# Performance work log

Hardware: AMD Instinct MI355X
Metric: run time of the kernel (lower is better)

The kernel has to match this reference:

```python
import jax, jax.numpy as jnp
import numpy as np
import math

D_MODEL = 1024
N_HEADS = 16
FFN_DIM = 4096
B, L = 8, 1024
LN_EPS = 1e-5


def setup_inputs() -> dict:
    key = jax.random.key(0)
    ks = jax.random.split(key, 16)
    s = 1.0 / math.sqrt(D_MODEL)
    sf = 1.0 / math.sqrt(FFN_DIM)
    # weights stored [in, out] (transposed vs torch nn.Linear)
    return {
        "x": jax.random.normal(ks[0], (B, L, D_MODEL), dtype=jnp.float32),
        "Wq": jax.random.normal(ks[1], (D_MODEL, D_MODEL), dtype=jnp.float32) * s,
        "bq": jnp.zeros((D_MODEL,), jnp.float32),
        "Wk": jax.random.normal(ks[2], (D_MODEL, D_MODEL), dtype=jnp.float32) * s,
        "bk": jnp.zeros((D_MODEL,), jnp.float32),
        "Wv": jax.random.normal(ks[3], (D_MODEL, D_MODEL), dtype=jnp.float32) * s,
        "bv": jnp.zeros((D_MODEL,), jnp.float32),
        "Wo": jax.random.normal(ks[4], (D_MODEL, D_MODEL), dtype=jnp.float32) * s,
        "bo": jnp.zeros((D_MODEL,), jnp.float32),
        "W1": jax.random.normal(ks[5], (D_MODEL, FFN_DIM), dtype=jnp.float32) * s,
        "b1": jnp.zeros((FFN_DIM,), jnp.float32),
        "W2": jax.random.normal(ks[6], (FFN_DIM, D_MODEL), dtype=jnp.float32) * sf,
        "b2": jnp.zeros((D_MODEL,), jnp.float32),
        "gamma": jnp.ones((D_MODEL,), jnp.float32),
        "beta": jnp.zeros((D_MODEL,), jnp.float32),
    }


def reference(x, Wq, bq, Wk, bk, Wv, bv, Wo, bo, W1, b1, W2, b2, gamma, beta):
    Bb, Ll, D = x.shape
    H = N_HEADS
    E = D // H
    scale = 1.0 / math.sqrt(E)
    # multi-head attention (dropout is identity in eval)
    q = (x @ Wq + bq).reshape(Bb, Ll, H, E)
    k = (x @ Wk + bk).reshape(Bb, Ll, H, E)
    v = (x @ Wv + bv).reshape(Bb, Ll, H, E)
    scores = jnp.einsum('blhe,bshe->bhls', q, k)  # [B,H,L,L]
    A = jax.nn.softmax(scale * scores, axis=-1)
    ctx = jnp.einsum('bhls,bshd->blhd', A, v).reshape(Bb, Ll, D)
    attn_out = ctx @ Wo + bo
    x = x + attn_out
    # FFN: conv1d kernel_size=1 == pointwise linear; exact (erf) GELU as in F.gelu
    h = jax.nn.gelu(x @ W1 + b1, approximate=False)
    x = x + (h @ W2 + b2)
    # LayerNorm
    mu = jnp.mean(x, axis=-1, keepdims=True)
    var = jnp.mean(jnp.square(x - mu), axis=-1, keepdims=True)
    out = (x - mu) * jax.lax.rsqrt(var + LN_EPS) * gamma + beta
    return out
```

## Files before the change

### kernel.cpp

```cpp
#include <hip/hip_runtime.h>
#include <cmath>

typedef __attribute__((ext_vector_type(8))) _Float16 half8;
typedef __attribute__((ext_vector_type(4))) _Float16 half4;
typedef __attribute__((ext_vector_type(4))) float f32x4;

__device__ __forceinline__ void glds16(const void* g, void* l) {
  __builtin_amdgcn_global_load_lds(
      (__attribute__((address_space(1))) const void*)g,
      (__attribute__((address_space(3))) void*)l, 16, 0, 0);
}

__device__ __forceinline__ float fast_erf(float x) {
  float ax = fabsf(x);
  float t = 1.0f / (1.0f + 0.3275911f * ax);
  float y = t * (0.254829592f +
            t * (-0.284496736f +
            t * (1.421413741f +
            t * (-1.453152027f + t * 1.061405429f))));
  float r = 1.0f - y * __expf(-ax * ax);
  return copysignf(r, x);
}

__global__ __launch_bounds__(256) void k_cvt(const float* __restrict__ in,
                                             _Float16* __restrict__ out) {
  int i = (blockIdx.x * 256 + threadIdx.x) * 8;
  const f32x4* p = (const f32x4*)(in + i);
  f32x4 a = p[0], b = p[1];
  half8 h;
  h[0] = (_Float16)a[0]; h[1] = (_Float16)a[1]; h[2] = (_Float16)a[2]; h[3] = (_Float16)a[3];
  h[4] = (_Float16)b[0]; h[5] = (_Float16)b[1]; h[6] = (_Float16)b[2]; h[7] = (_Float16)b[3];
  *(half8*)(out + i) = h;
}

__global__ __launch_bounds__(256) void k_wt(const float* __restrict__ W,
                                            _Float16* __restrict__ Wt, int K, int N) {
  __shared__ float t[32][33];
  int x = threadIdx.x & 31, y4 = (threadIdx.x >> 5) << 2;
  int n0 = blockIdx.x << 5, k0 = blockIdx.y << 5;
#pragma unroll
  for (int r = 0; r < 4; ++r) t[y4 + r][x] = W[(size_t)(k0 + y4 + r) * N + n0 + x];
  __syncthreads();
#pragma unroll
  for (int r = 0; r < 4; ++r) Wt[(size_t)(n0 + y4 + r) * K + k0 + x] = (_Float16)t[x][y4 + r];
}

__global__ void k_biascat(const float* __restrict__ a, const float* __restrict__ b,
                          const float* __restrict__ c, float* __restrict__ o) {
  int i = blockIdx.x * 256 + threadIdx.x;
  const float* s = i < 1024 ? a : (i < 2048 ? b : c);
  o[i] = s[i & 1023];
}

template <int BM, int EPI>
__global__ __launch_bounds__(512, 2) void k_gemm8(
    const _Float16* __restrict__ A, const _Float16* __restrict__ Bt,
    const float* __restrict__ bias, const float* __restrict__ res,
    float* __restrict__ outf, _Float16* __restrict__ outh, int M, int N, int K) {
  constexpr int MR = BM / 32;
  constexpr int MH2 = MR / 2;
  constexpr int AL = BM * 64;
  constexpr int BL = 256 * 64;
  constexpr int ABYTES = BM * 128;
  constexpr int BBYTES = 256 * 128;
  constexpr int AB2 = 2 * ABYTES;
  __shared__ _Float16 lds[2 * (AL + BL)];
  const char* ldsc = (const char*)lds;

  const int tid = threadIdx.x;
  const int lane = tid & 63;
  const int w = tid >> 6, wr = w >> 2, wc = w & 3;
  const int l15 = lane & 15, grp = lane >> 4;

  const int gx = gridDim.x;
  const int nwg = gx * gridDim.y;
  const int lid = blockIdx.y * gx + blockIdx.x;
  const int wid = (lid & 7) * (nwg >> 3) + (lid >> 3);
  const int m0 = (wid / gx) * BM, n0 = (wid % gx) * 256;

  const int m2 = (l15 >> 2) & 1, m01 = l15 & 3;
  const int chunk0 = (m2 << 2) | (grp ^ m01);
  const int aoff0 = wr * 2048 + l15 * 128 + chunk0 * 16;
  const int aoff1 = aoff0 ^ 64;
  const int boff0 = wc * 2048 + l15 * 128 + chunk0 * 16;
  const int boff1 = boff0 ^ 64;

  const int srow = tid >> 3;
  const int scs8 = ((tid & 7) ^ (srow & 7)) * 8;
  const int NK = K >> 6;

  f32x4 acc[MR][4] = {};
  half8 af[MH2][2], bf[2][2];

#define STG_A(J, MHH, KN)                                                      \
  _Pragma("unroll") for (int s = 0; s < BM / 128; ++s)                         \
      glds16(A + (size_t)(m0 + (MHH) * (BM / 2) + s * 64 + srow) * K +         \
                 (size_t)(KN)*64 + scs8,                                       \
             lds + (J)*AL + ((MHH) * (BM / 2) + s * 64) * 64 + tid * 8);
#define STG_B(J, NHH, KN)                                                      \
  _Pragma("unroll") for (int s = 0; s < 2; ++s)                                \
      glds16(Bt + (size_t)(n0 + (NHH)*128 + s * 64 + srow) * K +               \
                  (size_t)(KN)*64 + scs8,                                      \
             lds + 2 * AL + (J)*BL + ((NHH)*128 + s * 64) * 64 + tid * 8);

#define VM_C asm volatile("s_waitcnt vmcnt(2)" ::: "memory")
#define VM_NONE

#define PHASE(J, MHQ, NHQ, RA, RB, STGSTMT, VMSTMT)                            \
  {                                                                            \
    if constexpr (RA) {                                                        \
      _Pragma("unroll") for (int i = 0; i < MH2; ++i) {                        \
        af[i][0] = *(const half8*)(ldsc + (J)*ABYTES +                         \
                                   ((MHQ)*MH2 + i) * 4096 + aoff0);            \
        af[i][1] = *(const half8*)(ldsc + (J)*ABYTES +                         \
                                   ((MHQ)*MH2 + i) * 4096 + aoff1);            \
      }                                                                        \
    }                                                                          \
    if constexpr (RB) {                                                        \
      _Pragma("unroll") for (int n = 0; n < 2; ++n) {                          \
        bf[n][0] = *(const half8*)(ldsc + AB2 + (J)*BBYTES +                   \
                                   ((NHQ)*2 + n) * 8192 + boff0);              \
        bf[n][1] = *(const half8*)(ldsc + AB2 + (J)*BBYTES +                   \
                                   ((NHQ)*2 + n) * 8192 + boff1);              \
      }                                                                        \
    }                                                                          \
    STGSTMT;                                                                   \
    __builtin_amdgcn_s_barrier();                                              \
    asm volatile("s_waitcnt lgkmcnt(0)");                                      \
    __builtin_amdgcn_sched_barrier(0);                                         \
    __builtin_amdgcn_s_setprio(1);                                             \
    _Pragma("unroll") for (int ks = 0; ks < 2; ++ks)                           \
        _Pragma("unroll") for (int i = 0; i < MH2; ++i)                        \
            _Pragma("unroll") for (int n = 0; n < 2; ++n)                      \
                acc[(MHQ)*MH2 + i][(NHQ)*2 + n] =                              \
                    __builtin_amdgcn_mfma_f32_16x16x32_f16(                    \
                        af[i][ks], bf[n][ks], acc[(MHQ)*MH2 + i][(NHQ)*2 + n], \
                        0, 0, 0);                                              \
    __builtin_amdgcn_s_setprio(0);                                             \
    VMSTMT;                                                                    \
    __builtin_amdgcn_s_barrier();                                              \
  }

#define KTILE(J, KT)                                                           \
  {                                                                            \
    const int kn_ = ((KT) + 1 < NK) ? (KT) + 1 : NK - 1;                       \
    const int kn2_ = ((KT) + 2 < NK) ? (KT) + 2 : NK - 1;                      \
    PHASE(J, 0, 0, true, true, STG_A(1 - (J), 0, kn_), VM_NONE)                \
    PHASE(J, 0, 1, false, true, STG_A(1 - (J), 1, kn_), VM_NONE)               \
    PHASE(J, 1, 1, true, false, STG_B(1 - (J), 0, kn_), VM_NONE)               \
    PHASE(J, 1, 0, false, true, STG_B(J, 1, kn2_), VM_C)                       \
  }

  STG_A(0, 0, 0) STG_A(0, 1, 0) STG_B(0, 0, 0) STG_B(0, 1, 0)
  STG_B(1, 1, 1)
  VM_C;
  __builtin_amdgcn_s_barrier();

#pragma unroll 1
  for (int kt = 0; kt < NK; kt += 2) {
    KTILE(0, kt)
    KTILE(1, kt + 1)
  }
  asm volatile("s_waitcnt vmcnt(0)" ::: "memory");
#undef KTILE
#undef PHASE
#undef VM_C
#undef VM_NONE
#undef STG_A
#undef STG_B

  float bcol[4];
#pragma unroll
  for (int n = 0; n < 4; ++n) bcol[n] = bias[n0 + (n * 4 + wc) * 16 + l15];
#pragma unroll
  for (int m = 0; m < MR; ++m) {
#pragma unroll
    for (int rr = 0; rr < 4; ++rr) {
      const size_t row = m0 + (m * 2 + wr) * 16 + grp * 4 + rr;
#pragma unroll
      for (int n = 0; n < 4; ++n) {
        const int col = n0 + (n * 4 + wc) * 16 + l15;
        float v = acc[m][n][rr] + bcol[n];
        const size_t idx = row * N + col;
        if (EPI == 0) {
          outh[idx] = (_Float16)v;
        } else if (EPI == 1) {
          float t2 = v + res[idx];
          outf[idx] = t2;
          outh[idx] = (_Float16)t2;
        } else if (EPI == 2) {
          float g = 0.5f * v * (1.0f + fast_erf(v * 0.70710678118654752f));
          outh[idx] = (_Float16)g;
        } else {
          outf[idx] = v + res[idx];
        }
      }
    }
  }
}

template <int EPI>
__global__ __launch_bounds__(512, 2) void k_gemmf(
    const _Float16* __restrict__ A, const _Float16* __restrict__ Bt,
    const float* __restrict__ bias, const void* __restrict__ res,
    float* __restrict__ outf, _Float16* __restrict__ outh, int M, int N, int K) {
  constexpr int AL = 256 * 64, BL = 128 * 64;
  constexpr int ABY = 32768, BBY = 16384, BBASE = 3 * ABY;
  __shared__ _Float16 lds[3 * (AL + BL)];
  const char* ldsc = (const char*)lds;

  const int tid = threadIdx.x;
  const int lane = tid & 63;
  const int w = tid >> 6, wr = w >> 1, wc = w & 1;
  const int l15 = lane & 15, grp = lane >> 4;

  const int gx = gridDim.x;
  const int nwg = gx * gridDim.y;
  const int lid = blockIdx.y * gx + blockIdx.x;
  const int wid = (lid & 7) * (nwg >> 3) + (lid >> 3);
  const int m0 = (wid / gx) * 256, n0 = (wid % gx) * 128;

  const int m2 = (l15 >> 2) & 1, m01 = l15 & 3;
  const int c0 = ((m2 << 2) | (grp ^ m01)) * 16;
  const int aoff0 = wr * 2048 + l15 * 128 + c0;
  const int aoff1 = aoff0 ^ 64;
  const int boff0 = wc * 2048 + l15 * 128 + c0;
  const int boff1 = boff0 ^ 64;

  const int srow = tid >> 3;
  const int scs8 = ((tid & 7) ^ (srow & 7)) * 8;
  const int NK = K >> 6;

  const _Float16* aG = A + (size_t)(m0 + srow) * K + scs8;
  const _Float16* bG = Bt + (size_t)(n0 + srow) * K + scs8;

  f32x4 acc[4][4] = {};

#define FSTG_A(JJ, HH, KN)                                                     \
  _Pragma("unroll") for (int s = 0; s < 2; ++s)                                \
      glds16(aG + (size_t)((HH)*128 + s * 64) * K + (size_t)(KN)*64,           \
             lds + (JJ)*AL + ((HH)*128 + s * 64) * 64 + tid * 8);
#define FSTG_B(JJ, HH, KN)                                                     \
  glds16(bG + (size_t)((HH)*64) * K + (size_t)(KN)*64,                         \
         lds + 3 * AL + (JJ)*BL + (HH)*64 * 64 + tid * 8);

#define FPHASE(PA, PB, AO, BO, STGSTMT, VMSTMT)                                \
  {                                                                            \
    half8 af_[4], bf_[4];                                                      \
    _Pragma("unroll") for (int m = 0; m < 4; ++m)                              \
        af_[m] = *(const half8*)((PA) + m * 8192 + (AO));                      \
    _Pragma("unroll") for (int n = 0; n < 4; ++n)                              \
        bf_[n] = *(const half8*)((PB) + n * 4096 + (BO));                      \
    STGSTMT;                                                                   \
    __builtin_amdgcn_s_barrier();                                              \
    asm volatile("s_waitcnt lgkmcnt(0)");                                      \
    __builtin_amdgcn_sched_barrier(0);                                         \
    __builtin_amdgcn_s_setprio(1);                                             \
    _Pragma("unroll") for (int m = 0; m < 4; ++m)                              \
        _Pragma("unroll") for (int n = 0; n < 4; ++n)                          \
            acc[m][n] = __builtin_amdgcn_mfma_f32_16x16x32_f16(                \
                af_[m], bf_[n], acc[m][n], 0, 0, 0);                           \
    __builtin_amdgcn_s_setprio(0);                                             \
    VMSTMT;                                                                    \
    __builtin_amdgcn_s_barrier();                                              \
  }

  FSTG_A(0, 0, 0) FSTG_A(0, 1, 0) FSTG_B(0, 0, 0) FSTG_B(0, 1, 0)
  FSTG_A(1, 0, 1) FSTG_A(1, 1, 1) FSTG_B(1, 0, 1) FSTG_B(1, 1, 1)
  asm volatile("s_waitcnt vmcnt(6)" ::: "memory");
  __builtin_amdgcn_s_barrier();

  int j = 0, j2 = 2;
#pragma unroll 1
  for (int kt = 0; kt < NK; ++kt) {
    const int kn = (kt + 2 < NK) ? kt + 2 : NK - 1;
    const char* pa = ldsc + j * ABY;
    const char* pb = ldsc + BBASE + j * BBY;
    FPHASE(pa, pb, aoff0, boff0, { FSTG_A(j2, 0, kn) FSTG_B(j2, 0, kn) }, )
    FPHASE(pa, pb, aoff1, boff1, { FSTG_A(j2, 1, kn) FSTG_B(j2, 1, kn) },
           asm volatile("s_waitcnt vmcnt(6)" ::: "memory");)
    j = (j == 2) ? 0 : j + 1;
    j2 = (j2 == 2) ? 0 : j2 + 1;
  }
  asm volatile("s_waitcnt vmcnt(0)" ::: "memory");
#undef FPHASE
#undef FSTG_A
#undef FSTG_B

  float bcol[4];
#pragma unroll
  for (int n = 0; n < 4; ++n) bcol[n] = bias[n0 + (n * 2 + wc) * 16 + l15];
#pragma unroll
  for (int m = 0; m < 4; ++m) {
#pragma unroll
    for (int rr = 0; rr < 4; ++rr) {
      const size_t row = m0 + (m * 4 + wr) * 16 + grp * 4 + rr;
#pragma unroll
      for (int n = 0; n < 4; ++n) {
        const int col = n0 + (n * 2 + wc) * 16 + l15;
        float v = acc[m][n][rr] + bcol[n];
        const size_t idx = row * N + col;
        if (EPI == 0) {
          outh[idx] = (_Float16)v;
        } else if (EPI == 1) {
          float t2 = v + ((const float*)res)[idx];
          outh[idx] = (_Float16)t2;
        } else if (EPI == 2) {
          float g = 0.5f * v * (1.0f + fast_erf(v * 0.70710678118654752f));
          outh[idx] = (_Float16)g;
        } else {
          float t2 = v + (float)((const _Float16*)res)[idx];
          outf[idx] = t2;
        }
      }
    }
  }
}

__global__ __launch_bounds__(256) void k_vt(const _Float16* __restrict__ qkv,
                                            _Float16* __restrict__ Vt) {
  __shared__ _Float16 t[64 * 66];
  const int tid = threadIdx.x;
  const int bh = blockIdx.y, b = bh >> 4, h = bh & 15;
  const int s0 = blockIdx.x << 6;
#pragma unroll
  for (int p = 0; p < 2; ++p) {
    int lin = p * 256 + tid;
    int s = lin >> 3, c8 = lin & 7;
    half8 v = *(const half8*)&qkv[(size_t)(b * 1024 + s0 + s) * 3072 + 2048 + h * 64 + c8 * 8];
    union { half8 h8; unsigned u[4]; } u;
    u.h8 = v;
    unsigned* d = (unsigned*)&t[s * 66 + c8 * 8];
#pragma unroll
    for (int k = 0; k < 4; ++k) d[k] = u.u[k];
  }
  __syncthreads();
#pragma unroll
  for (int p = 0; p < 2; ++p) {
    int lin = p * 256 + tid;
    int e = lin >> 3, c8 = lin & 7;
    half8 v;
#pragma unroll
    for (int j = 0; j < 8; ++j) v[j] = t[(c8 * 8 + j) * 66 + e];
    *(half8*)&Vt[(size_t)(bh * 64 + e) * 1024 + s0 + c8 * 8] = v;
  }
}

__global__ __launch_bounds__(256) void k_attn(const _Float16* __restrict__ qkv,
                                              const _Float16* __restrict__ Vt,
                                              _Float16* __restrict__ ctx) {
  __shared__ _Float16 Ks[128 * 64];
  __shared__ _Float16 Vs[64 * 128];
  __shared__ _Float16 Ps[4][16 * 136];
  const int tid = threadIdx.x;
  const int lane = tid & 63, w = tid >> 6;
  const int l15 = lane & 15, grp = lane >> 4;
  const int bh = blockIdx.y, b = bh >> 4, h = bh & 15;
  const int q0 = blockIdx.x << 6;
  const float CSC = 0.125f * 1.44269504088896f;

  half8 qf[2];
  {
    const _Float16* qp = qkv + (size_t)(b * 1024 + q0 + w * 16 + l15) * 3072 + h * 64 + grp * 8;
    qf[0] = *(const half8*)qp;
    qf[1] = *(const half8*)(qp + 32);
  }
  f32x4 octx[4] = {};
  float mrun = -1e30f, lrun = 0.f;

  for (int kt = 0; kt < 8; ++kt) {
    const int s0 = kt * 128;
#pragma unroll
    for (int i = 0; i < 4; ++i) {
      {
        int srow = i * 32 + (tid >> 3);
        int c8 = (tid & 7) ^ (srow & 7);
        glds16(qkv + (size_t)(b * 1024 + s0 + srow) * 3072 + 1024 + h * 64 + c8 * 8,
               Ks + w * 512 + i * 2048);
      }
      {
        int erow = i * 16 + (tid >> 4);
        int c16 = (tid & 15) ^ (erow & 7);
        glds16(Vt + (size_t)(bh * 64 + erow) * 1024 + s0 + c16 * 8,
               Vs + w * 512 + i * 2048);
      }
    }
    __syncthreads();
    f32x4 sacc[8] = {};
#pragma unroll
    for (int ks = 0; ks < 2; ++ks)
#pragma unroll
      for (int f = 0; f < 8; ++f) {
        int srow = f * 16 + l15;
        half8 kf = *(const half8*)&Ks[srow * 64 + ((ks * 32 + grp * 8) ^ ((srow & 7) * 8))];
        sacc[f] = __builtin_amdgcn_mfma_f32_16x16x32_f16(kf, qf[ks], sacc[f], 0, 0, 0);
      }
    float sv[8][4];
    float tmax = -1e30f;
#pragma unroll
    for (int f = 0; f < 8; ++f)
#pragma unroll
      for (int r = 0; r < 4; ++r) {
        float v = sacc[f][r] * CSC;
        sv[f][r] = v;
        tmax = fmaxf(tmax, v);
      }
    tmax = fmaxf(tmax, __shfl_xor(tmax, 16));
    tmax = fmaxf(tmax, __shfl_xor(tmax, 32));
    float mnew = fmaxf(mrun, tmax);
    float corr = exp2f(mrun - mnew);
    float tsum = 0.f;
#pragma unroll
    for (int f = 0; f < 8; ++f)
#pragma unroll
      for (int r = 0; r < 4; ++r) {
        float pv = exp2f(sv[f][r] - mnew);
        sv[f][r] = pv;
        tsum += pv;
      }
    tsum += __shfl_xor(tsum, 16);
    tsum += __shfl_xor(tsum, 32);
    lrun = lrun * corr + tsum;
    mrun = mnew;
#pragma unroll
    for (int r = 0; r < 4; ++r) {
      float cq = __shfl(corr, (lane & 48) + grp * 4 + r);
#pragma unroll
      for (int jf = 0; jf < 4; ++jf) octx[jf][r] *= cq;
    }
#pragma unroll
    for (int f = 0; f < 8; ++f) {
      half4 pk;
      pk[0] = (_Float16)sv[f][0]; pk[1] = (_Float16)sv[f][1];
      pk[2] = (_Float16)sv[f][2]; pk[3] = (_Float16)sv[f][3];
      *(half4*)&Ps[w][l15 * 136 + f * 16 + grp * 4] = pk;
    }
#pragma unroll
    for (int ks2 = 0; ks2 < 4; ++ks2) {
      half8 pa = *(const half8*)&Ps[w][l15 * 136 + ks2 * 32 + grp * 8];
#pragma unroll
      for (int jf = 0; jf < 4; ++jf) {
        int erow = jf * 16 + l15;
        half8 vb = *(const half8*)&Vs[erow * 128 + ((ks2 * 32 + grp * 8) ^ ((erow & 7) * 8))];
        octx[jf] = __builtin_amdgcn_mfma_f32_16x16x32_f16(pa, vb, octx[jf], 0, 0, 0);
      }
    }
    __syncthreads();
  }
#pragma unroll
  for (int r = 0; r < 4; ++r) {
    float lq = __shfl(lrun, (lane & 48) + grp * 4 + r);
    float inv = 1.0f / lq;
    const size_t row = b * 1024 + q0 + w * 16 + grp * 4 + r;
#pragma unroll
    for (int jf = 0; jf < 4; ++jf)
      ctx[row * 1024 + h * 64 + jf * 16 + l15] = (_Float16)(octx[jf][r] * inv);
  }
}

__global__ __launch_bounds__(256) void k_ln(const float* xin, const float* __restrict__ gamma,
                                            const float* __restrict__ beta, float* out) {
  __shared__ float red[8];
  const int tid = threadIdx.x;
  const size_t row = blockIdx.x;
  f32x4 v = *(const f32x4*)&xin[row * 1024 + tid * 4];
  float s = v[0] + v[1] + v[2] + v[3];
  float s2 = v[0] * v[0] + v[1] * v[1] + v[2] * v[2] + v[3] * v[3];
#pragma unroll
  for (int o = 32; o >= 1; o >>= 1) {
    s += __shfl_xor(s, o);
    s2 += __shfl_xor(s2, o);
  }
  if ((tid & 63) == 0) { red[tid >> 6] = s; red[4 + (tid >> 6)] = s2; }
  __syncthreads();
  s = red[0] + red[1] + red[2] + red[3];
  s2 = red[4] + red[5] + red[6] + red[7];
  float mu = s * (1.0f / 1024.0f);
  float var = s2 * (1.0f / 1024.0f) - mu * mu;
  float rs = rsqrtf(var + 1e-5f);
  f32x4 g = *(const f32x4*)&gamma[tid * 4];
  f32x4 bt = *(const f32x4*)&beta[tid * 4];
  f32x4 o4;
#pragma unroll
  for (int r = 0; r < 4; ++r) o4[r] = (v[r] - mu) * rs * g[r] + bt[r];
  *(f32x4*)&out[row * 1024 + tid * 4] = o4;
}

extern "C" void kernel_launch(void* const* d_in, const int* in_sizes, int n_in,
                              void* d_out, int out_size, void* d_ws, size_t ws_size,
                              hipStream_t stream) {
  (void)in_sizes; (void)n_in; (void)out_size; (void)ws_size;
  const float* x  = (const float*)d_in[0];
  const float* Wq = (const float*)d_in[1];  const float* bq = (const float*)d_in[2];
  const float* Wk = (const float*)d_in[3];  const float* bk = (const float*)d_in[4];
  const float* Wv = (const float*)d_in[5];  const float* bv = (const float*)d_in[6];
  const float* Wo = (const float*)d_in[7];  const float* bo = (const float*)d_in[8];
  const float* W1 = (const float*)d_in[9];  const float* b1 = (const float*)d_in[10];
  const float* W2 = (const float*)d_in[11]; const float* b2 = (const float*)d_in[12];
  const float* gamma = (const float*)d_in[13];
  const float* beta  = (const float*)d_in[14];
  float* out = (float*)d_out;

  char* p = (char*)d_ws;
  _Float16* xb    = (_Float16*)p;  p += (size_t)16 << 20;
  _Float16* qkv   = (_Float16*)p;
  _Float16* hbuf  = (_Float16*)p;  p += (size_t)48 << 20;
  _Float16* Vt    = (_Float16*)p;  p += (size_t)16 << 20;
  _Float16* Wqkvt = (_Float16*)p;  p += (size_t)3072 * 1024 * 2;
  _Float16* Wot   = (_Float16*)p;  p += (size_t)1024 * 1024 * 2;
  _Float16* W1t   = (_Float16*)p;  p += (size_t)4096 * 1024 * 2;
  _Float16* W2t   = (_Float16*)p;  p += (size_t)4096 * 1024 * 2;
  float*    bqkv  = (float*)p;     p += (size_t)3072 * 4;
  _Float16* x1b   = (_Float16*)p;  p += (size_t)16 << 20;
  _Float16* ctx   = xb;

  k_cvt<<<4096, 256, 0, stream>>>(x, xb);
  k_wt<<<dim3(32, 32), 256, 0, stream>>>(Wq, Wqkvt, 1024, 1024);
  k_wt<<<dim3(32, 32), 256, 0, stream>>>(Wk, Wqkvt + 1024 * 1024, 1024, 1024);
  k_wt<<<dim3(32, 32), 256, 0, stream>>>(Wv, Wqkvt + 2048 * 1024, 1024, 1024);
  k_wt<<<dim3(32, 32), 256, 0, stream>>>(Wo, Wot, 1024, 1024);
  k_wt<<<dim3(128, 32), 256, 0, stream>>>(W1, W1t, 1024, 4096);
  k_wt<<<dim3(32, 128), 256, 0, stream>>>(W2, W2t, 4096, 1024);
  k_biascat<<<12, 256, 0, stream>>>(bq, bk, bv, bqkv);

  k_gemmf<0><<<dim3(24, 32), 512, 0, stream>>>(xb, Wqkvt, bqkv, nullptr, nullptr, qkv,
                                               8192, 3072, 1024);
  k_vt<<<dim3(16, 128), 256, 0, stream>>>(qkv, Vt);
  k_attn<<<dim3(16, 128), 256, 0, stream>>>(qkv, Vt, ctx);
  k_gemmf<1><<<dim3(8, 32), 512, 0, stream>>>(ctx, Wot, bo, x, nullptr, x1b,
                                              8192, 1024, 1024);
  k_gemm8<256, 2><<<dim3(16, 32), 512, 0, stream>>>(x1b, W1t, b1, nullptr, nullptr, hbuf,
                                                    8192, 4096, 1024);
  k_gemmf<4><<<dim3(8, 32), 512, 0, stream>>>(hbuf, W2t, b2, x1b, out, nullptr,
                                              8192, 1024, 4096);
  k_ln<<<8192, 256, 0, stream>>>(out, gamma, beta, out);
}
```

Baseline: 360.3 us.

## Fuse V transpose into QKV GEMM epilogue and double query rows per attention block

The QKV GEMM gets a new epilogue mode that writes the V columns directly in transposed [b,h,e,s] layout, so the separate k_vt transpose kernel and its extra pass over V are removed. The attention kernel now handles 128 query rows per block (two 64-row sub-tiles), reusing each K/V tile loaded into LDS twice and halving the grid. The order of the A/B staging loads in the GEMM pipeline phases is also swapped. Costs: the transposed V stores are 8-byte scattered writes, and attention has more registers per thread and fewer blocks in flight.

After: 361.0 us. Within noise of the previous version (+0.2%).

```diff
diff --git a/kernel.cpp b/kernel.cpp
--- a/kernel.cpp
+++ b/kernel.cpp
@@ -146,12 +146,12 @@
     const int kn_ = ((KT) + 1 < NK) ? (KT) + 1 : NK - 1;                       \
     const int kn2_ = ((KT) + 2 < NK) ? (KT) + 2 : NK - 1;                      \
     PHASE(J, 0, 0, true, true, STG_A(1 - (J), 0, kn_), VM_NONE)                \
-    PHASE(J, 0, 1, false, true, STG_A(1 - (J), 1, kn_), VM_NONE)               \
-    PHASE(J, 1, 1, true, false, STG_B(1 - (J), 0, kn_), VM_NONE)               \
+    PHASE(J, 0, 1, false, true, STG_B(1 - (J), 0, kn_), VM_NONE)               \
+    PHASE(J, 1, 1, true, false, STG_A(1 - (J), 1, kn_), VM_NONE)               \
     PHASE(J, 1, 0, false, true, STG_B(J, 1, kn2_), VM_C)                       \
   }
 
-  STG_A(0, 0, 0) STG_A(0, 1, 0) STG_B(0, 0, 0) STG_B(0, 1, 0)
+  STG_A(0, 0, 0) STG_B(0, 0, 0) STG_A(0, 1, 0) STG_B(0, 1, 0)
   STG_B(1, 1, 1)
   VM_C;
   __builtin_amdgcn_s_barrier();
@@ -290,6 +290,30 @@
   float bcol[4];
 #pragma unroll
   for (int n = 0; n < 4; ++n) bcol[n] = bias[n0 + (n * 2 + wc) * 16 + l15];
+  if (EPI == 5) {
+    _Float16* vt = (_Float16*)outf;
+#pragma unroll
+    for (int m = 0; m < 4; ++m) {
+#pragma unroll
+      for (int n = 0; n < 4; ++n) {
+        const int col = n0 + (n * 2 + wc) * 16 + l15;
+        const size_t row0 = m0 + (m * 4 + wr) * 16 + grp * 4;
+        if (col < 2048) {
+#pragma unroll
+          for (int rr = 0; rr < 4; ++rr)
+            outh[(row0 + rr) * (size_t)N + col] = (_Float16)(acc[m][n][rr] + bcol[n]);
+        } else {
+          const int b = (int)(row0 >> 10), s = (int)(row0 & 1023);
+          const int cv = col - 2048, hh = cv >> 6, e = cv & 63;
+          half4 pk;
+#pragma unroll
+          for (int rr = 0; rr < 4; ++rr) pk[rr] = (_Float16)(acc[m][n][rr] + bcol[n]);
+          *(half4*)&vt[((size_t)((b << 4) | hh) * 64 + e) * 1024 + s] = pk;
+        }
+      }
+    }
+    return;
+  }
 #pragma unroll
   for (int m = 0; m < 4; ++m) {
 #pragma unroll
@@ -317,35 +341,6 @@
   }
 }
 
-__global__ __launch_bounds__(256) void k_vt(const _Float16* __restrict__ qkv,
-                                            _Float16* __restrict__ Vt) {
-  __shared__ _Float16 t[64 * 66];
-  const int tid = threadIdx.x;
-  const int bh = blockIdx.y, b = bh >> 4, h = bh & 15;
-  const int s0 = blockIdx.x << 6;
-#pragma unroll
-  for (int p = 0; p < 2; ++p) {
-    int lin = p * 256 + tid;
-    int s = lin >> 3, c8 = lin & 7;
-    half8 v = *(const half8*)&qkv[(size_t)(b * 1024 + s0 + s) * 3072 + 2048 + h * 64 + c8 * 8];
-    union { half8 h8; unsigned u[4]; } u;
-    u.h8 = v;
-    unsigned* d = (unsigned*)&t[s * 66 + c8 * 8];
-#pragma unroll
-    for (int k = 0; k < 4; ++k) d[k] = u.u[k];
-  }
-  __syncthreads();
-#pragma unroll
-  for (int p = 0; p < 2; ++p) {
-    int lin = p * 256 + tid;
-    int e = lin >> 3, c8 = lin & 7;
-    half8 v;
-#pragma unroll
-    for (int j = 0; j < 8; ++j) v[j] = t[(c8 * 8 + j) * 66 + e];
-    *(half8*)&Vt[(size_t)(bh * 64 + e) * 1024 + s0 + c8 * 8] = v;
-  }
-}
-
 __global__ __launch_bounds__(256) void k_attn(const _Float16* __restrict__ qkv,
                                               const _Float16* __restrict__ Vt,
                                               _Float16* __restrict__ ctx) {
@@ -356,17 +351,19 @@
   const int lane = tid & 63, w = tid >> 6;
   const int l15 = lane & 15, grp = lane >> 4;
   const int bh = blockIdx.y, b = bh >> 4, h = bh & 15;
-  const int q0 = blockIdx.x << 6;
+  const int q0 = blockIdx.x << 7;
   const float CSC = 0.125f * 1.44269504088896f;
 
-  half8 qf[2];
-  {
-    const _Float16* qp = qkv + (size_t)(b * 1024 + q0 + w * 16 + l15) * 3072 + h * 64 + grp * 8;
-    qf[0] = *(const half8*)qp;
-    qf[1] = *(const half8*)(qp + 32);
-  }
-  f32x4 octx[4] = {};
-  float mrun = -1e30f, lrun = 0.f;
+  half8 qf[2][2];
+#pragma unroll
+  for (int qs = 0; qs < 2; ++qs) {
+    const _Float16* qp =
+        qkv + (size_t)(b * 1024 + q0 + qs * 64 + w * 16 + l15) * 3072 + h * 64 + grp * 8;
+    qf[qs][0] = *(const half8*)qp;
+    qf[qs][1] = *(const half8*)(qp + 32);
+  }
+  f32x4 octx[2][4] = {};
+  float mrun[2] = {-1e30f, -1e30f}, lrun[2] = {0.f, 0.f};
 
   for (int kt = 0; kt < 8; ++kt) {
     const int s0 = kt * 128;
@@ -386,75 +383,81 @@
       }
     }
     __syncthreads();
-    f32x4 sacc[8] = {};
-#pragma unroll
-    for (int ks = 0; ks < 2; ++ks)
+#pragma unroll
+    for (int qs = 0; qs < 2; ++qs) {
+      f32x4 sacc[8] = {};
+#pragma unroll
+      for (int ks = 0; ks < 2; ++ks)
+#pragma unroll
+        for (int f = 0; f < 8; ++f) {
+          int srow = f * 16 + l15;
+          half8 kf = *(const half8*)&Ks[srow * 64 + ((ks * 32 + grp * 8) ^ ((srow & 7) * 8))];
+          sacc[f] = __builtin_amdgcn_mfma_f32_16x16x32_f16(kf, qf[qs][ks], sacc[f], 0, 0, 0);
+        }
+      float sv[8][4];
+      float tmax = -1e30f;
+#pragma unroll
+      for (int f = 0; f < 8; ++f)
+#pragma unroll
+        for (int r = 0; r < 4; ++r) {
+          float v = sacc[f][r] * CSC;
+          sv[f][r] = v;
+          tmax = fmaxf(tmax, v);
+        }
+      tmax = fmaxf(tmax, __shfl_xor(tmax, 16));
+      tmax = fmaxf(tmax, __shfl_xor(tmax, 32));
+      float mnew = fmaxf(mrun[qs], tmax);
+      float corr = exp2f(mrun[qs] - mnew);
+      float tsum = 0.f;
+#pragma unroll
+      for (int f = 0; f < 8; ++f)
+#pragma unroll
+        for (int r = 0; r < 4; ++r) {
+          float pv = exp2f(sv[f][r] - mnew);
+          sv[f][r] = pv;
+          tsum += pv;
+        }
+      tsum += __shfl_xor(tsum, 16);
+      tsum += __shfl_xor(tsum, 32);
+      lrun[qs] = lrun[qs] * corr + tsum;
+      mrun[qs] = mnew;
+#pragma unroll
+      for (int r = 0; r < 4; ++r) {
+        float cq = __shfl(corr, (lane & 48) + grp * 4 + r);
+#pragma unroll
+        for (int jf = 0; jf < 4; ++jf) octx[qs][jf][r] *= cq;
+      }
 #pragma unroll
       for (int f = 0; f < 8; ++f) {
-        int srow = f * 16 + l15;
-        half8 kf = *(const half8*)&Ks[srow * 64 + ((ks * 32 + grp * 8) ^ ((srow & 7) * 8))];
-        sacc[f] = __builtin_amdgcn_mfma_f32_16x16x32_f16(kf, qf[ks], sacc[f], 0, 0, 0);
-      }
-    float sv[8][4];
-    float tmax = -1e30f;
-#pragma unroll
-    for (int f = 0; f < 8; ++f)
-#pragma unroll
-      for (int r = 0; r < 4; ++r) {
-        float v = sacc[f][r] * CSC;
-        sv[f][r] = v;
-        tmax = fmaxf(tmax, v);
-      }
-    tmax = fmaxf(tmax, __shfl_xor(tmax, 16));
-    tmax = fmaxf(tmax, __shfl_xor(tmax, 32));
-    float mnew = fmaxf(mrun, tmax);
-    float corr = exp2f(mrun - mnew);
-    float tsum = 0.f;
-#pragma unroll
-    for (int f = 0; f < 8; ++f)
-#pragma unroll
-      for (int r = 0; r < 4; ++r) {
-        float pv = exp2f(sv[f][r] - mnew);
-        sv[f][r] = pv;
-        tsum += pv;
-      }
-    tsum += __shfl_xor(tsum, 16);
-    tsum += __shfl_xor(tsum, 32);
-    lrun = lrun * corr + tsum;
-    mrun = mnew;
-#pragma unroll
-    for (int r = 0; r < 4; ++r) {
-      float cq = __shfl(corr, (lane & 48) + grp * 4 + r);
-#pragma unroll
-      for (int jf = 0; jf < 4; ++jf) octx[jf][r] *= cq;
-    }
-#pragma unroll
-    for (int f = 0; f < 8; ++f) {
-      half4 pk;
-      pk[0] = (_Float16)sv[f][0]; pk[1] = (_Float16)sv[f][1];
-      pk[2] = (_Float16)sv[f][2]; pk[3] = (_Float16)sv[f][3];
-      *(half4*)&Ps[w][l15 * 136 + f * 16 + grp * 4] = pk;
-    }
-#pragma unroll
-    for (int ks2 = 0; ks2 < 4; ++ks2) {
-      half8 pa = *(const half8*)&Ps[w][l15 * 136 + ks2 * 32 + grp * 8];
-#pragma unroll
-      for (int jf = 0; jf < 4; ++jf) {
-        int erow = jf * 16 + l15;
-        half8 vb = *(const half8*)&Vs[erow * 128 + ((ks2 * 32 + grp * 8) ^ ((erow & 7) * 8))];
-        octx[jf] = __builtin_amdgcn_mfma_f32_16x16x32_f16(pa, vb, octx[jf], 0, 0, 0);
+        half4 pk;
+        pk[0] = (_Float16)sv[f][0]; pk[1] = (_Float16)sv[f][1];
+        pk[2] = (_Float16)sv[f][2]; pk[3] = (_Float16)sv[f][3];
+        *(half4*)&Ps[w][l15 * 136 + f * 16 + grp * 4] = pk;
+      }
+#pragma unroll
+      for (int ks2 = 0; ks2 < 4; ++ks2) {
+        half8 pa = *(const half8*)&Ps[w][l15 * 136 + ks2 * 32 + grp * 8];
+#pragma unroll
+        for (int jf = 0; jf < 4; ++jf) {
+          int erow = jf * 16 + l15;
+          half8 vb = *(const half8*)&Vs[erow * 128 + ((ks2 * 32 + grp * 8) ^ ((erow & 7) * 8))];
+          octx[qs][jf] = __builtin_amdgcn_mfma_f32_16x16x32_f16(pa, vb, octx[qs][jf], 0, 0, 0);
+        }
       }
     }
     __syncthreads();
   }
 #pragma unroll
-  for (int r = 0; r < 4; ++r) {
-    float lq = __shfl(lrun, (lane & 48) + grp * 4 + r);
-    float inv = 1.0f / lq;
-    const size_t row = b * 1024 + q0 + w * 16 + grp * 4 + r;
-#pragma unroll
-    for (int jf = 0; jf < 4; ++jf)
-      ctx[row * 1024 + h * 64 + jf * 16 + l15] = (_Float16)(octx[jf][r] * inv);
+  for (int qs = 0; qs < 2; ++qs) {
+#pragma unroll
+    for (int r = 0; r < 4; ++r) {
+      float lq = __shfl(lrun[qs], (lane & 48) + grp * 4 + r);
+      float inv = 1.0f / lq;
+      const size_t row = b * 1024 + q0 + qs * 64 + w * 16 + grp * 4 + r;
+#pragma unroll
+      for (int jf = 0; jf < 4; ++jf)
+        ctx[row * 1024 + h * 64 + jf * 16 + l15] = (_Float16)(octx[qs][jf][r] * inv);
+    }
   }
 }
 
@@ -523,10 +526,9 @@
   k_wt<<<dim3(32, 128), 256, 0, stream>>>(W2, W2t, 4096, 1024);
   k_biascat<<<12, 256, 0, stream>>>(bq, bk, bv, bqkv);
 
-  k_gemmf<0><<<dim3(24, 32), 512, 0, stream>>>(xb, Wqkvt, bqkv, nullptr, nullptr, qkv,
+  k_gemmf<5><<<dim3(24, 32), 512, 0, stream>>>(xb, Wqkvt, bqkv, nullptr, (float*)Vt, qkv,
                                                8192, 3072, 1024);
-  k_vt<<<dim3(16, 128), 256, 0, stream>>>(qkv, Vt);
-  k_attn<<<dim3(16, 128), 256, 0, stream>>>(qkv, Vt, ctx);
+  k_attn<<<dim3(8, 128), 256, 0, stream>>>(qkv, Vt, ctx);
   k_gemmf<1><<<dim3(8, 32), 512, 0, stream>>>(ctx, Wot, bo, x, nullptr, x1b,
                                               8192, 1024, 1024);
   k_gemm8<256, 2><<<dim3(16, 32), 512, 0, stream>>>(x1b, W1t, b1, nullptr, nullptr, hbuf,
```
